# Kernel optimization log

Measured on AMD Instinct MI355X. Metric: run time of the kernel, lower is better.

## Reference

```python
import jax, jax.numpy as jnp
import numpy as np

B, S, DIN, DQK, DV = 4, 4096, 1024, 64, 64


def setup_inputs() -> dict:
    key = jax.random.key(0)
    ks = jax.random.split(key, 10)
    inv = 1.0 / np.sqrt(DIN)
    return {
        "query": jax.random.normal(ks[0], (B, S, DIN), dtype=jnp.float32),
        "key": jax.random.normal(ks[1], (B, S, DIN), dtype=jnp.float32),
        "value": jax.random.normal(ks[2], (B, S, DIN), dtype=jnp.float32),
        "mask": jnp.ones((B, S, S), dtype=jnp.int32),
        "Wq": jax.random.uniform(ks[3], (DIN, DQK), jnp.float32, -inv, inv),
        "bq": jax.random.uniform(ks[4], (DQK,), jnp.float32, -inv, inv),
        "Wk": jax.random.uniform(ks[5], (DIN, DQK), jnp.float32, -inv, inv),
        "bk": jax.random.uniform(ks[6], (DQK,), jnp.float32, -inv, inv),
        "Wv": jax.random.uniform(ks[7], (DIN, DV), jnp.float32, -inv, inv),
        "bv": jax.random.uniform(ks[8], (DV,), jnp.float32, -inv, inv),
    }


def reference(query, key, value, mask, Wq, bq, Wk, bk, Wv, bv):
    q = jnp.einsum("bsd,de->bse", query, Wq) + bq  # [B,S,DQK]
    k = jnp.einsum("bsd,de->bse", key, Wk) + bk    # [B,S,DQK]
    v = jnp.einsum("bsd,de->bse", value, Wv) + bv  # [B,S,DV]
    # faithful nonstandard scale: sqrt(dim_qk + 1e-8)
    scale = jnp.sqrt(jnp.float32(q.shape[-1]) + 1e-8)
    scores = jnp.einsum("bqe,bke->bqk", q, k) / scale  # [B,S,S]
    scores = jnp.where(mask == 0, jnp.float32(-jnp.inf), scores)
    attn = jax.nn.softmax(scores, axis=-1)
    return jnp.einsum("bqk,bkv->bqv", attn, v)  # [B,S,DV]
```

## Files before the change

kernel.cpp:

```cpp
#include <hip/hip_runtime.h>

#define NB 4
#define NS 4096
#define NDIN 1024
#define ND 64

typedef __attribute__((ext_vector_type(4))) float f32x4;
typedef __attribute__((ext_vector_type(8))) short s16x8;
typedef __attribute__((ext_vector_type(4))) short s16x4;

__device__ __forceinline__ unsigned short f2bf(float f) {
  union { float f; unsigned u; } x; x.f = f;
  unsigned r = x.u + 0x7fffu + ((x.u >> 16) & 1u);
  return (unsigned short)(r >> 16);
}

__device__ __forceinline__ unsigned cvtpk(float lo, float hi) {
  unsigned r;
  asm("v_cvt_pk_bf16_f32 %0, %1, %2" : "=v"(r) : "v"(lo), "v"(hi));
  return r;
}

__device__ __forceinline__ void gload16(const void* g, void* l) {
  __builtin_amdgcn_global_load_lds(
      (const __attribute__((address_space(1))) void*)g,
      (__attribute__((address_space(3))) void*)l, 16, 0, 0);
}

__global__ __launch_bounds__(256) void prep_w_kernel(
    const float* __restrict__ Wq, const float* __restrict__ Wk,
    const float* __restrict__ Wv, unsigned short* __restrict__ wt) {
  int idx = blockIdx.x * 256 + threadIdx.x;
  int m = idx >> 16;
  int r = idx & 65535;
  int c = r >> 10;
  int k = r & 1023;
  const float* W = (m == 0) ? Wq : (m == 1) ? Wk : Wv;
  wt[idx] = f2bf(W[k * ND + c]);
}

__global__ __launch_bounds__(256, 4) void proj_kernel(
    const float* __restrict__ Xq, const float* __restrict__ Xk, const float* __restrict__ Xv,
    const float* __restrict__ bq, const float* __restrict__ bk, const float* __restrict__ bv,
    const unsigned short* __restrict__ wt_all,
    unsigned short* __restrict__ q_o, unsigned short* __restrict__ k_o,
    unsigned short* __restrict__ vt_o) {
  __shared__ float xsm[2][64 * 64];

  const int y = blockIdx.y;
  const float* __restrict__ X = (y == 0) ? Xq : (y == 1) ? Xk : Xv;
  const float* __restrict__ bias = (y == 0) ? bq : (y == 1) ? bk : bv;
  const unsigned short* __restrict__ wt = wt_all + y * (ND * NDIN);
  const int row0 = blockIdx.x * 64;
  const int tid = threadIdx.x;
  const int lane = tid & 63;
  const int w = tid >> 6;
  const int ql = lane & 15;
  const int grp = lane >> 4;
  const int swz = (ql & 7) << 4;

  int osrc[4];
  #pragma unroll
  for (int j = 0; j < 4; ++j) {
    const int o = w * 4096 + j * 1024 + lane * 16;
    const int row = o >> 8, c = o & 255;
    osrc[j] = row * 4096 + (c ^ ((row & 7) << 4));
  }

  const char* xg = (const char*)(X + (size_t)row0 * NDIN);
  auto stageX = [&](int kk, int buf) {
    const char* src = xg + kk * 256;
    char* dst = (char*)xsm + buf * 16384 + w * 4096;
    #pragma unroll
    for (int j = 0; j < 4; ++j) gload16(src + osrc[j], dst + j * 1024);
  };

  f32x4 acc[4] = {};

  stageX(0, 0);
  asm volatile("s_waitcnt vmcnt(0)" ::: "memory");
  __syncthreads();

  for (int kk = 0; kk < 16; ++kk) {
    const int cur = kk & 1;
    if (kk < 15) stageX(kk + 1, cur ^ 1);
    __builtin_amdgcn_sched_barrier(0);

    const char* xr = (const char*)xsm + cur * 16384 + (16 * w + ql) * 256;
    #pragma unroll
    for (int half = 0; half < 2; ++half) {
      const f32x4 a0 = *reinterpret_cast<const f32x4*>(
          xr + ((half * 128 + grp * 32) ^ swz));
      const f32x4 a1 = *reinterpret_cast<const f32x4*>(
          xr + ((half * 128 + grp * 32 + 16) ^ swz));
      union { s16x8 v; unsigned u[4]; } a;
      a.u[0] = cvtpk(a0[0], a0[1]);
      a.u[1] = cvtpk(a0[2], a0[3]);
      a.u[2] = cvtpk(a1[0], a1[1]);
      a.u[3] = cvtpk(a1[2], a1[3]);
      const unsigned short* wk = wt + kk * 64 + half * 32 + grp * 8;
      #pragma unroll
      for (int nt = 0; nt < 4; ++nt) {
        const s16x8 bfr = *reinterpret_cast<const s16x8*>(wk + (size_t)(ql + 16 * nt) * NDIN);
        acc[nt] = __builtin_amdgcn_mfma_f32_16x16x32_bf16(a.v, bfr, acc[nt], 0, 0, 0);
      }
    }

    asm volatile("s_waitcnt vmcnt(0)" ::: "memory");
    __syncthreads();
  }

  const int b = row0 >> 12;
  const int s0 = row0 & 4095;
  #pragma unroll
  for (int nt = 0; nt < 4; ++nt) {
    const int col = ql + 16 * nt;
    const float bia = bias[col];
    #pragma unroll
    for (int r = 0; r < 4; ++r) {
      const int rr = 16 * w + grp * 4 + r;
      const unsigned short h = f2bf(acc[nt][r] + bia);
      if (y == 0) {
        q_o[(size_t)(row0 + rr) * ND + col] = h;
      } else if (y == 1) {
        k_o[(size_t)(row0 + rr) * ND + col] = h;
      } else {
        vt_o[(size_t)b * ND * NS + (size_t)col * NS + (s0 + rr)] = h;
      }
    }
  }
}

__global__ __launch_bounds__(256, 4) void attn_kernel(
    const unsigned short* __restrict__ qm, const unsigned short* __restrict__ km,
    const unsigned short* __restrict__ vt, const int* __restrict__ mask,
    float* __restrict__ opart, float* __restrict__ ml) {
  __shared__ unsigned short ksm[2][4096];
  __shared__ unsigned short vsm[2][4096];
  __shared__ unsigned short psm[4096];

  const int bid = blockIdx.x;
  const int combo = bid & 15;
  const int qblk = bid >> 4;
  const int b = combo >> 2;
  const int split = combo & 3;
  const int q0 = qblk * 64;
  const int kv00 = split * 1024;

  const int tid = threadIdx.x;
  const int lane = tid & 63;
  const int w = tid >> 6;
  const int ql = lane & 15;
  const int grp = lane >> 4;

  const int swz = (ql & 7) << 4;
  const int fK0 = ql * 128 + ((grp * 16) ^ swz);
  const int fK1 = ql * 128 + ((grp * 16 + 64) ^ swz);

  int oK0, oK1, oV0, oV1;
  {
    const int o0 = w * 2048 + lane * 16;
    const int o1 = o0 + 1024;
    oK0 = o0 ^ (((o0 >> 7) & 7) << 4);
    oK1 = o1 ^ (((o1 >> 7) & 7) << 4);
    const int d0 = o0 >> 7, c0 = o0 & 127;
    const int d1 = o1 >> 7, c1 = o1 & 127;
    oV0 = d0 * 8192 + (c0 ^ ((d0 & 7) << 4));
    oV1 = d1 * 8192 + (c1 ^ ((d1 & 7) << 4));
  }

  const char* kg = (const char*)(km + (size_t)b * NS * ND + (size_t)kv00 * ND);
  const char* vg = (const char*)(vt + (size_t)b * ND * NS + kv00);
  char* const klds = (char*)&ksm[0][0] + w * 2048;
  char* const vlds = (char*)&vsm[0][0] + w * 2048;
  char* const pw = (char*)&psm[0] + w * 2048;

  const size_t qrow = (size_t)(b * NS + q0 + w * 16 + ql) * ND;
  const s16x8 qf0 = *reinterpret_cast<const s16x8*>(qm + qrow + grp * 8);
  const s16x8 qf1 = *reinterpret_cast<const s16x8*>(qm + qrow + 32 + grp * 8);

  const int* __restrict__ mrow =
      mask + (size_t)(b * NS + q0 + w * 16 + ql) * NS + kv00;

  f32x4 acc[4] = {};
  float m_i = -INFINITY;
  float l_i = 0.f;
  const float CSC = 0.18033688011112042f;
  const float THR = 11.54f;

  auto stage = [&](int t, int buf) {
    const char* kt = kg + (size_t)t * 8192;
    const char* vtb = vg + (size_t)t * 128;
    gload16(kt + oK0, klds + buf * 8192);
    gload16(kt + oK1, klds + buf * 8192 + 1024);
    gload16(vtb + oV0, vlds + buf * 8192);
    gload16(vtb + oV1, vlds + buf * 8192 + 1024);
  };

  stage(0, 0);
  int4 mc0 = *reinterpret_cast<const int4*>(mrow + grp * 4);
  int4 mc1 = *reinterpret_cast<const int4*>(mrow + 16 + grp * 4);
  int4 mc2 = *reinterpret_cast<const int4*>(mrow + 32 + grp * 4);
  int4 mc3 = *reinterpret_cast<const int4*>(mrow + 48 + grp * 4);
  asm volatile("s_waitcnt vmcnt(0)" ::: "memory");
  __syncthreads();

  for (int t = 0; t < 16; ++t) {
    const int cur = t & 1;
    if (t < 15) stage(t + 1, cur ^ 1);
    __builtin_amdgcn_sched_barrier(0);

    const char* kread = (const char*)&ksm[0][0] + cur * 8192;
    const char* vread = (const char*)&vsm[0][0] + cur * 8192;

    f32x4 s4[4];
    __builtin_amdgcn_s_setprio(1);
    #pragma unroll
    for (int mt = 0; mt < 4; ++mt) {
      const s16x8 kf0 = *reinterpret_cast<const s16x8*>(kread + mt * 2048 + fK0);
      const s16x8 kf1 = *reinterpret_cast<const s16x8*>(kread + mt * 2048 + fK1);
      f32x4 s = {0.f, 0.f, 0.f, 0.f};
      s = __builtin_amdgcn_mfma_f32_16x16x32_bf16(kf0, qf0, s, 0, 0, 0);
      s = __builtin_amdgcn_mfma_f32_16x16x32_bf16(kf1, qf1, s, 0, 0, 0);
      s4[mt] = s;
    }
    __builtin_amdgcn_s_setprio(0);

    float sc[16];
    {
      const int4 m0 = mc0, m1 = mc1, m2 = mc2, m3 = mc3;
      sc[0]  = (m0.x != 0) ? s4[0][0] * CSC : -1e30f;
      sc[1]  = (m0.y != 0) ? s4[0][1] * CSC : -1e30f;
      sc[2]  = (m0.z != 0) ? s4[0][2] * CSC : -1e30f;
      sc[3]  = (m0.w != 0) ? s4[0][3] * CSC : -1e30f;
      sc[4]  = (m1.x != 0) ? s4[1][0] * CSC : -1e30f;
      sc[5]  = (m1.y != 0) ? s4[1][1] * CSC : -1e30f;
      sc[6]  = (m1.z != 0) ? s4[1][2] * CSC : -1e30f;
      sc[7]  = (m1.w != 0) ? s4[1][3] * CSC : -1e30f;
      sc[8]  = (m2.x != 0) ? s4[2][0] * CSC : -1e30f;
      sc[9]  = (m2.y != 0) ? s4[2][1] * CSC : -1e30f;
      sc[10] = (m2.z != 0) ? s4[2][2] * CSC : -1e30f;
      sc[11] = (m2.w != 0) ? s4[2][3] * CSC : -1e30f;
      sc[12] = (m3.x != 0) ? s4[3][0] * CSC : -1e30f;
      sc[13] = (m3.y != 0) ? s4[3][1] * CSC : -1e30f;
      sc[14] = (m3.z != 0) ? s4[3][2] * CSC : -1e30f;
      sc[15] = (m3.w != 0) ? s4[3][3] * CSC : -1e30f;
    }
    if (t < 15) {
      const int* mn = mrow + (t + 1) * 64;
      mc0 = *reinterpret_cast<const int4*>(mn + grp * 4);
      mc1 = *reinterpret_cast<const int4*>(mn + 16 + grp * 4);
      mc2 = *reinterpret_cast<const int4*>(mn + 32 + grp * 4);
      mc3 = *reinterpret_cast<const int4*>(mn + 48 + grp * 4);
    }

    float t0 = fmaxf(fmaxf(sc[0], sc[1]), fmaxf(sc[2], sc[3]));
    float t1 = fmaxf(fmaxf(sc[4], sc[5]), fmaxf(sc[6], sc[7]));
    float t2 = fmaxf(fmaxf(sc[8], sc[9]), fmaxf(sc[10], sc[11]));
    float t3 = fmaxf(fmaxf(sc[12], sc[13]), fmaxf(sc[14], sc[15]));
    float tm = fmaxf(fmaxf(t0, t1), fmaxf(t2, t3));
    tm = fmaxf(tm, __shfl_xor(tm, 16));
    tm = fmaxf(tm, __shfl_xor(tm, 32));
    if (!__all(tm <= m_i + THR)) {
      const float nm = fmaxf(m_i, tm);
      const float alpha = exp2f(m_i - nm);
      #pragma unroll
      for (int r = 0; r < 4; ++r) {
        const float ar = __shfl(alpha, grp * 4 + r);
        acc[0][r] *= ar;
        acc[1][r] *= ar;
        acc[2][r] *= ar;
        acc[3][r] *= ar;
      }
      l_i *= alpha;
      m_i = nm;
    }
    #pragma unroll
    for (int r = 0; r < 16; ++r) sc[r] = exp2f(sc[r] - m_i);
    float u0 = (sc[0] + sc[1]) + (sc[2] + sc[3]);
    float u1 = (sc[4] + sc[5]) + (sc[6] + sc[7]);
    float u2 = (sc[8] + sc[9]) + (sc[10] + sc[11]);
    float u3 = (sc[12] + sc[13]) + (sc[14] + sc[15]);
    float ssum = (u0 + u1) + (u2 + u3);
    ssum += __shfl_xor(ssum, 16);
    ssum += __shfl_xor(ssum, 32);
    l_i += ssum;

    #pragma unroll
    for (int mt = 0; mt < 4; ++mt) {
      uint2 pk;
      pk.x = cvtpk(sc[4 * mt + 0], sc[4 * mt + 1]);
      pk.y = cvtpk(sc[4 * mt + 2], sc[4 * mt + 3]);
      *reinterpret_cast<uint2*>(pw + ql * 128 + ((mt * 32 + grp * 8) ^ swz)) = pk;
    }

    #pragma unroll
    for (int ks = 0; ks < 2; ++ks) {
      const s16x8 pa = *reinterpret_cast<const s16x8*>(
          pw + ql * 128 + ((ks * 64 + grp * 16) ^ swz));
      const int fV = ks ? fK1 : fK0;
      __builtin_amdgcn_s_setprio(1);
      #pragma unroll
      for (int nt = 0; nt < 4; ++nt) {
        const s16x8 vb = *reinterpret_cast<const s16x8*>(vread + nt * 2048 + fV);
        acc[nt] = __builtin_amdgcn_mfma_f32_16x16x32_bf16(pa, vb, acc[nt], 0, 0, 0);
      }
      __builtin_amdgcn_s_setprio(0);
    }

    asm volatile("s_waitcnt vmcnt(16)" ::: "memory");
    __syncthreads();
  }

  const int qg = b * NS + q0 + w * 16;
  float* obase = opart + ((size_t)split * (NB * NS) + qg) * 64;
  #pragma unroll
  for (int nt = 0; nt < 4; ++nt) {
    #pragma unroll
    for (int r = 0; r < 4; ++r) {
      obase[(size_t)(grp * 4 + r) * 64 + ql + 16 * nt] = acc[nt][r];
    }
  }
  if (grp == 0) {
    float* mlp = ml + ((size_t)split * (NB * NS) + qg + ql) * 2;
    mlp[0] = m_i;
    mlp[1] = l_i;
  }
}

__global__ __launch_bounds__(256) void combine_kernel(
    const float* __restrict__ opart, const float* __restrict__ ml,
    float* __restrict__ out) {
  const int idx = blockIdx.x * 256 + threadIdx.x;
  const int q = idx >> 4;
  const int dc = (idx & 15) * 4;
  const float2 a0 = *reinterpret_cast<const float2*>(ml + (size_t)q * 2);
  const float2 a1 = *reinterpret_cast<const float2*>(ml + (size_t)(16384 + q) * 2);
  const float2 a2 = *reinterpret_cast<const float2*>(ml + (size_t)(32768 + q) * 2);
  const float2 a3 = *reinterpret_cast<const float2*>(ml + (size_t)(49152 + q) * 2);
  const float M = fmaxf(fmaxf(a0.x, a1.x), fmaxf(a2.x, a3.x));
  const float w0 = exp2f(a0.x - M), w1 = exp2f(a1.x - M);
  const float w2 = exp2f(a2.x - M), w3 = exp2f(a3.x - M);
  const float inv = 1.f / (a0.y * w0 + a1.y * w1 + a2.y * w2 + a3.y * w3);
  f32x4 o = (*reinterpret_cast<const f32x4*>(opart + (size_t)q * 64 + dc)) * w0;
  o += (*reinterpret_cast<const f32x4*>(opart + ((size_t)16384 + q) * 64 + dc)) * w1;
  o += (*reinterpret_cast<const f32x4*>(opart + ((size_t)32768 + q) * 64 + dc)) * w2;
  o += (*reinterpret_cast<const f32x4*>(opart + ((size_t)49152 + q) * 64 + dc)) * w3;
  o *= inv;
  *reinterpret_cast<f32x4*>(out + (size_t)q * 64 + dc) = o;
}

extern "C" void kernel_launch(void* const* d_in, const int* in_sizes, int n_in,
                              void* d_out, int out_size, void* d_ws, size_t ws_size,
                              hipStream_t stream) {
  const float* query = (const float*)d_in[0];
  const float* key   = (const float*)d_in[1];
  const float* value = (const float*)d_in[2];
  const int*   mask  = (const int*)d_in[3];
  const float* Wq = (const float*)d_in[4];
  const float* bq = (const float*)d_in[5];
  const float* Wk = (const float*)d_in[6];
  const float* bk = (const float*)d_in[7];
  const float* Wv = (const float*)d_in[8];
  const float* bv = (const float*)d_in[9];
  float* out = (float*)d_out;

  char* ws = (char*)d_ws;
  unsigned short* wt    = (unsigned short*)(ws);
  unsigned short* qb    = (unsigned short*)(ws + 393216);
  unsigned short* kb    = (unsigned short*)(ws + 2490368);
  unsigned short* vtb   = (unsigned short*)(ws + 4587520);
  float*          opart = (float*)(ws + 6684672);
  float*          mlb   = (float*)(ws + 23461888);

  prep_w_kernel<<<dim3(768), dim3(256), 0, stream>>>(Wq, Wk, Wv, wt);
  proj_kernel<<<dim3(256, 3), dim3(256), 0, stream>>>(query, key, value,
                                                      bq, bk, bv, wt, qb, kb, vtb);
  attn_kernel<<<dim3(1024), dim3(256), 0, stream>>>(qb, kb, vtb, mask, opart, mlb);
  combine_kernel<<<dim3(1024), dim3(256), 0, stream>>>(opart, mlb, out);
}
```

Before: 151.1 us.

## Stage projection weights in LDS and unroll attention loop by two with mask prefetch

The projection kernel now double-buffers the bf16 weight tile in swizzled LDS through async global-to-LDS loads, instead of reading B fragments straight from global memory inside the MFMA loop. The attention loop is unrolled by two so buffer indices become compile-time, and the mask for the next tile is prefetched into a double-buffered register array at the start of each step rather than after use. The last-iteration wait and barrier are skipped. Both kernels drop their occupancy hint from 4 to 3 waves per SIMD, which gives more registers and LDS headroom but may lower latency hiding.

```diff
diff --git a/kernel.cpp b/kernel.cpp
--- a/kernel.cpp
+++ b/kernel.cpp
@@ -39,18 +39,19 @@
   wt[idx] = f2bf(W[k * ND + c]);
 }
 
-__global__ __launch_bounds__(256, 4) void proj_kernel(
+__global__ __launch_bounds__(256, 3) void proj_kernel(
     const float* __restrict__ Xq, const float* __restrict__ Xk, const float* __restrict__ Xv,
     const float* __restrict__ bq, const float* __restrict__ bk, const float* __restrict__ bv,
     const unsigned short* __restrict__ wt_all,
     unsigned short* __restrict__ q_o, unsigned short* __restrict__ k_o,
     unsigned short* __restrict__ vt_o) {
-  __shared__ float xsm[2][64 * 64];
+  __shared__ float xsm[2][4096];
+  __shared__ unsigned short wsm[2][4096];
 
   const int y = blockIdx.y;
   const float* __restrict__ X = (y == 0) ? Xq : (y == 1) ? Xk : Xv;
   const float* __restrict__ bias = (y == 0) ? bq : (y == 1) ? bk : bv;
-  const unsigned short* __restrict__ wt = wt_all + y * (ND * NDIN);
+  const char* __restrict__ wg = (const char*)(wt_all + y * (ND * NDIN));
   const int row0 = blockIdx.x * 64;
   const int tid = threadIdx.x;
   const int lane = tid & 63;
@@ -59,12 +60,19 @@
   const int grp = lane >> 4;
   const int swz = (ql & 7) << 4;
 
-  int osrc[4];
+  int osrcX[4];
   #pragma unroll
   for (int j = 0; j < 4; ++j) {
     const int o = w * 4096 + j * 1024 + lane * 16;
     const int row = o >> 8, c = o & 255;
-    osrc[j] = row * 4096 + (c ^ ((row & 7) << 4));
+    osrcX[j] = row * 4096 + (c ^ ((row & 7) << 4));
+  }
+  int osrcW[2];
+  #pragma unroll
+  for (int j = 0; j < 2; ++j) {
+    const int o = w * 2048 + j * 1024 + lane * 16;
+    const int row = o >> 7, c = o & 127;
+    osrcW[j] = row * 2048 + (c ^ ((row & 7) << 4));
   }
 
   const char* xg = (const char*)(X + (size_t)row0 * NDIN);
@@ -72,21 +80,35 @@
     const char* src = xg + kk * 256;
     char* dst = (char*)xsm + buf * 16384 + w * 4096;
     #pragma unroll
-    for (int j = 0; j < 4; ++j) gload16(src + osrc[j], dst + j * 1024);
+    for (int j = 0; j < 4; ++j) gload16(src + osrcX[j], dst + j * 1024);
   };
+  auto stageW = [&](int kk, int buf) {
+    const char* src = wg + kk * 128;
+    char* dst = (char*)wsm + buf * 8192 + w * 2048;
+    gload16(src + osrcW[0], dst);
+    gload16(src + osrcW[1], dst + 1024);
+  };
+
+  const int fw0 = (grp * 16) ^ swz;
+  const int fw1 = (grp * 16 + 64) ^ swz;
 
   f32x4 acc[4] = {};
 
   stageX(0, 0);
+  stageW(0, 0);
   asm volatile("s_waitcnt vmcnt(0)" ::: "memory");
   __syncthreads();
 
   for (int kk = 0; kk < 16; ++kk) {
     const int cur = kk & 1;
-    if (kk < 15) stageX(kk + 1, cur ^ 1);
+    if (kk < 15) {
+      stageX(kk + 1, cur ^ 1);
+      stageW(kk + 1, cur ^ 1);
+    }
     __builtin_amdgcn_sched_barrier(0);
 
     const char* xr = (const char*)xsm + cur * 16384 + (16 * w + ql) * 256;
+    const char* wr = (const char*)wsm + cur * 8192;
     #pragma unroll
     for (int half = 0; half < 2; ++half) {
       const f32x4 a0 = *reinterpret_cast<const f32x4*>(
@@ -98,10 +120,10 @@
       a.u[1] = cvtpk(a0[2], a0[3]);
       a.u[2] = cvtpk(a1[0], a1[1]);
       a.u[3] = cvtpk(a1[2], a1[3]);
-      const unsigned short* wk = wt + kk * 64 + half * 32 + grp * 8;
+      const int fw = half ? fw1 : fw0;
       #pragma unroll
       for (int nt = 0; nt < 4; ++nt) {
-        const s16x8 bfr = *reinterpret_cast<const s16x8*>(wk + (size_t)(ql + 16 * nt) * NDIN);
+        const s16x8 bfr = *reinterpret_cast<const s16x8*>(wr + (ql + 16 * nt) * 128 + fw);
         acc[nt] = __builtin_amdgcn_mfma_f32_16x16x32_bf16(a.v, bfr, acc[nt], 0, 0, 0);
       }
     }
@@ -131,7 +153,7 @@
   }
 }
 
-__global__ __launch_bounds__(256, 4) void attn_kernel(
+__global__ __launch_bounds__(256, 3) void attn_kernel(
     const unsigned short* __restrict__ qm, const unsigned short* __restrict__ km,
     const unsigned short* __restrict__ vt, const int* __restrict__ mask,
     float* __restrict__ opart, float* __restrict__ ml) {
@@ -197,119 +219,119 @@
     gload16(vtb + oV1, vlds + buf * 8192 + 1024);
   };
 
+  int4 mc[2][4];
+
   stage(0, 0);
-  int4 mc0 = *reinterpret_cast<const int4*>(mrow + grp * 4);
-  int4 mc1 = *reinterpret_cast<const int4*>(mrow + 16 + grp * 4);
-  int4 mc2 = *reinterpret_cast<const int4*>(mrow + 32 + grp * 4);
-  int4 mc3 = *reinterpret_cast<const int4*>(mrow + 48 + grp * 4);
+  {
+    mc[0][0] = *reinterpret_cast<const int4*>(mrow + grp * 4);
+    mc[0][1] = *reinterpret_cast<const int4*>(mrow + 16 + grp * 4);
+    mc[0][2] = *reinterpret_cast<const int4*>(mrow + 32 + grp * 4);
+    mc[0][3] = *reinterpret_cast<const int4*>(mrow + 48 + grp * 4);
+  }
   asm volatile("s_waitcnt vmcnt(0)" ::: "memory");
   __syncthreads();
 
-  for (int t = 0; t < 16; ++t) {
-    const int cur = t & 1;
-    if (t < 15) stage(t + 1, cur ^ 1);
-    __builtin_amdgcn_sched_barrier(0);
-
-    const char* kread = (const char*)&ksm[0][0] + cur * 8192;
-    const char* vread = (const char*)&vsm[0][0] + cur * 8192;
-
-    f32x4 s4[4];
-    __builtin_amdgcn_s_setprio(1);
+  for (int tt = 0; tt < 16; tt += 2) {
     #pragma unroll
-    for (int mt = 0; mt < 4; ++mt) {
-      const s16x8 kf0 = *reinterpret_cast<const s16x8*>(kread + mt * 2048 + fK0);
-      const s16x8 kf1 = *reinterpret_cast<const s16x8*>(kread + mt * 2048 + fK1);
-      f32x4 s = {0.f, 0.f, 0.f, 0.f};
-      s = __builtin_amdgcn_mfma_f32_16x16x32_bf16(kf0, qf0, s, 0, 0, 0);
-      s = __builtin_amdgcn_mfma_f32_16x16x32_bf16(kf1, qf1, s, 0, 0, 0);
-      s4[mt] = s;
+    for (int ph = 0; ph < 2; ++ph) {
+      const int t = tt + ph;
+      const int cur = ph;
+
+      if (t < 15) {
+        stage(t + 1, cur ^ 1);
+        const int* mn = mrow + (t + 1) * 64;
+        mc[ph ^ 1][0] = *reinterpret_cast<const int4*>(mn + grp * 4);
+        mc[ph ^ 1][1] = *reinterpret_cast<const int4*>(mn + 16 + grp * 4);
+        mc[ph ^ 1][2] = *reinterpret_cast<const int4*>(mn + 32 + grp * 4);
+        mc[ph ^ 1][3] = *reinterpret_cast<const int4*>(mn + 48 + grp * 4);
+      }
+      __builtin_amdgcn_sched_barrier(0);
+
+      const char* kread = (const char*)&ksm[0][0] + cur * 8192;
+      const char* vread = (const char*)&vsm[0][0] + cur * 8192;
+
+      f32x4 s4[4];
+      __builtin_amdgcn_s_setprio(1);
+      #pragma unroll
+      for (int mt = 0; mt < 4; ++mt) {
+        const s16x8 kf0 = *reinterpret_cast<const s16x8*>(kread + mt * 2048 + fK0);
+        const s16x8 kf1 = *reinterpret_cast<const s16x8*>(kread + mt * 2048 + fK1);
+        f32x4 s = {0.f, 0.f, 0.f, 0.f};
+        s = __builtin_amdgcn_mfma_f32_16x16x32_bf16(kf0, qf0, s, 0, 0, 0);
+        s = __builtin_amdgcn_mfma_f32_16x16x32_bf16(kf1, qf1, s, 0, 0, 0);
+        s4[mt] = s;
+      }
+      __builtin_amdgcn_s_setprio(0);
+
+      float sc[16];
+      #pragma unroll
+      for (int mt = 0; mt < 4; ++mt) {
+        const int4 m = mc[ph][mt];
+        sc[4 * mt + 0] = (m.x != 0) ? s4[mt][0] * CSC : -1e30f;
+        sc[4 * mt + 1] = (m.y != 0) ? s4[mt][1] * CSC : -1e30f;
+        sc[4 * mt + 2] = (m.z != 0) ? s4[mt][2] * CSC : -1e30f;
+        sc[4 * mt + 3] = (m.w != 0) ? s4[mt][3] * CSC : -1e30f;
+      }
+
+      float t0 = fmaxf(fmaxf(sc[0], sc[1]), fmaxf(sc[2], sc[3]));
+      float t1 = fmaxf(fmaxf(sc[4], sc[5]), fmaxf(sc[6], sc[7]));
+      float t2 = fmaxf(fmaxf(sc[8], sc[9]), fmaxf(sc[10], sc[11]));
+      float t3 = fmaxf(fmaxf(sc[12], sc[13]), fmaxf(sc[14], sc[15]));
+      float tm = fmaxf(fmaxf(t0, t1), fmaxf(t2, t3));
+      tm = fmaxf(tm, __shfl_xor(tm, 16));
+      tm = fmaxf(tm, __shfl_xor(tm, 32));
+      if (!__all(tm <= m_i + THR)) {
+        const float nm = fmaxf(m_i, tm);
+        const float alpha = exp2f(m_i - nm);
+        #pragma unroll
+        for (int r = 0; r < 4; ++r) {
+          const float ar = __shfl(alpha, grp * 4 + r);
+          acc[0][r] *= ar;
+          acc[1][r] *= ar;
+          acc[2][r] *= ar;
+          acc[3][r] *= ar;
+        }
+        l_i *= alpha;
+        m_i = nm;
+      }
+      #pragma unroll
+      for (int r = 0; r < 16; ++r) sc[r] = exp2f(sc[r] - m_i);
+      float u0 = (sc[0] + sc[1]) + (sc[2] + sc[3]);
+      float u1 = (sc[4] + sc[5]) + (sc[6] + sc[7]);
+      float u2 = (sc[8] + sc[9]) + (sc[10] + sc[11]);
+      float u3 = (sc[12] + sc[13]) + (sc[14] + sc[15]);
+      float ssum = (u0 + u1) + (u2 + u3);
+      ssum += __shfl_xor(ssum, 16);
+      ssum += __shfl_xor(ssum, 32);
+      l_i += ssum;
+
+      #pragma unroll
+      for (int mt = 0; mt < 4; ++mt) {
+        uint2 pk;
+        pk.x = cvtpk(sc[4 * mt + 0], sc[4 * mt + 1]);
+        pk.y = cvtpk(sc[4 * mt + 2], sc[4 * mt + 3]);
+        *reinterpret_cast<uint2*>(pw + ql * 128 + ((mt * 32 + grp * 8) ^ swz)) = pk;
+      }
+
+      #pragma unroll
+      for (int ks = 0; ks < 2; ++ks) {
+        const s16x8 pa = *reinterpret_cast<const s16x8*>(
+            pw + ql * 128 + ((ks * 64 + grp * 16) ^ swz));
+        const int fV = ks ? fK1 : fK0;
+        __builtin_amdgcn_s_setprio(1);
+        #pragma unroll
+        for (int nt = 0; nt < 4; ++nt) {
+          const s16x8 vb = *reinterpret_cast<const s16x8*>(vread + nt * 2048 + fV);
+          acc[nt] = __builtin_amdgcn_mfma_f32_16x16x32_bf16(pa, vb, acc[nt], 0, 0, 0);
+        }
+        __builtin_amdgcn_s_setprio(0);
+      }
+
+      if (t < 15) {
+        asm volatile("s_waitcnt vmcnt(16)" ::: "memory");
+        __syncthreads();
+      }
     }
-    __builtin_amdgcn_s_setprio(0);
-
-    float sc[16];
-    {
-      const int4 m0 = mc0, m1 = mc1, m2 = mc2, m3 = mc3;
-      sc[0]  = (m0.x != 0) ? s4[0][0] * CSC : -1e30f;
-      sc[1]  = (m0.y != 0) ? s4[0][1] * CSC : -1e30f;
-      sc[2]  = (m0.z != 0) ? s4[0][2] * CSC : -1e30f;
-      sc[3]  = (m0.w != 0) ? s4[0][3] * CSC : -1e30f;
-      sc[4]  = (m1.x != 0) ? s4[1][0] * CSC : -1e30f;
-      sc[5]  = (m1.y != 0) ? s4[1][1] * CSC : -1e30f;
-      sc[6]  = (m1.z != 0) ? s4[1][2] * CSC : -1e30f;
-      sc[7]  = (m1.w != 0) ? s4[1][3] * CSC : -1e30f;
-      sc[8]  = (m2.x != 0) ? s4[2][0] * CSC : -1e30f;
-      sc[9]  = (m2.y != 0) ? s4[2][1] * CSC : -1e30f;
-      sc[10] = (m2.z != 0) ? s4[2][2] * CSC : -1e30f;
-      sc[11] = (m2.w != 0) ? s4[2][3] * CSC : -1e30f;
-      sc[12] = (m3.x != 0) ? s4[3][0] * CSC : -1e30f;
-      sc[13] = (m3.y != 0) ? s4[3][1] * CSC : -1e30f;
-      sc[14] = (m3.z != 0) ? s4[3][2] * CSC : -1e30f;
-      sc[15] = (m3.w != 0) ? s4[3][3] * CSC : -1e30f;
-    }
-    if (t < 15) {
-      const int* mn = mrow + (t + 1) * 64;
-      mc0 = *reinterpret_cast<const int4*>(mn + grp * 4);
-      mc1 = *reinterpret_cast<const int4*>(mn + 16 + grp * 4);
-      mc2 = *reinterpret_cast<const int4*>(mn + 32 + grp * 4);
-      mc3 = *reinterpret_cast<const int4*>(mn + 48 + grp * 4);
-    }
-
-    float t0 = fmaxf(fmaxf(sc[0], sc[1]), fmaxf(sc[2], sc[3]));
-    float t1 = fmaxf(fmaxf(sc[4], sc[5]), fmaxf(sc[6], sc[7]));
-    float t2 = fmaxf(fmaxf(sc[8], sc[9]), fmaxf(sc[10], sc[11]));
-    float t3 = fmaxf(fmaxf(sc[12], sc[13]), fmaxf(sc[14], sc[15]));
-    float tm = fmaxf(fmaxf(t0, t1), fmaxf(t2, t3));
-    tm = fmaxf(tm, __shfl_xor(tm, 16));
-    tm = fmaxf(tm, __shfl_xor(tm, 32));
-    if (!__all(tm <= m_i + THR)) {
-      const float nm = fmaxf(m_i, tm);
-      const float alpha = exp2f(m_i - nm);
-      #pragma unroll
-      for (int r = 0; r < 4; ++r) {
-        const float ar = __shfl(alpha, grp * 4 + r);
-        acc[0][r] *= ar;
-        acc[1][r] *= ar;
-        acc[2][r] *= ar;
-        acc[3][r] *= ar;
-      }
-      l_i *= alpha;
-      m_i = nm;
-    }
-    #pragma unroll
-    for (int r = 0; r < 16; ++r) sc[r] = exp2f(sc[r] - m_i);
-    float u0 = (sc[0] + sc[1]) + (sc[2] + sc[3]);
-    float u1 = (sc[4] + sc[5]) + (sc[6] + sc[7]);
-    float u2 = (sc[8] + sc[9]) + (sc[10] + sc[11]);
-    float u3 = (sc[12] + sc[13]) + (sc[14] + sc[15]);
-    float ssum = (u0 + u1) + (u2 + u3);
-    ssum += __shfl_xor(ssum, 16);
-    ssum += __shfl_xor(ssum, 32);
-    l_i += ssum;
-
-    #pragma unroll
-    for (int mt = 0; mt < 4; ++mt) {
-      uint2 pk;
-      pk.x = cvtpk(sc[4 * mt + 0], sc[4 * mt + 1]);
-      pk.y = cvtpk(sc[4 * mt + 2], sc[4 * mt + 3]);
-      *reinterpret_cast<uint2*>(pw + ql * 128 + ((mt * 32 + grp * 8) ^ swz)) = pk;
-    }
-
-    #pragma unroll
-    for (int ks = 0; ks < 2; ++ks) {
-      const s16x8 pa = *reinterpret_cast<const s16x8*>(
-          pw + ql * 128 + ((ks * 64 + grp * 16) ^ swz));
-      const int fV = ks ? fK1 : fK0;
-      __builtin_amdgcn_s_setprio(1);
-      #pragma unroll
-      for (int nt = 0; nt < 4; ++nt) {
-        const s16x8 vb = *reinterpret_cast<const s16x8*>(vread + nt * 2048 + fV);
-        acc[nt] = __builtin_amdgcn_mfma_f32_16x16x32_bf16(pa, vb, acc[nt], 0, 0, 0);
-      }
-      __builtin_amdgcn_s_setprio(0);
-    }
-
-    asm volatile("s_waitcnt vmcnt(16)" ::: "memory");
-    __syncthreads();
   }
 
   const int qg = b * NS + q0 + w * 16;
```

Result: faster. 132.0 us (-12.6%).
